# Optimization experiments

Hardware: AMD Instinct MI355X
Metric: run time of the kernel (lower is better)

Reference implementation:

```python
import jax, jax.numpy as jnp
import numpy as np

TEMPERATURE = 8.0  # sqrt(d_k), d_k = 64


def setup_inputs() -> dict:
    key = jax.random.key(0)
    kq, kk, kv = jax.random.split(key, 3)
    BH, N, D = 16, 4096, 64  # batch*heads, seq_len, head_dim
    q = jax.random.normal(kq, (BH, N, D), dtype=jnp.float32)
    k = jax.random.normal(kk, (BH, N, D), dtype=jnp.float32)
    v = jax.random.normal(kv, (BH, N, D), dtype=jnp.float32)
    # causal mask: True means masked (filled with -inf), broadcast over BH
    mask = jnp.triu(jnp.ones((N, N), dtype=jnp.bool_), k=1)[None, :, :]
    return {"q": q, "k": k, "v": v, "mask": mask}


def reference(q, k, v, mask):
    # attn = q @ k^T / temperature, masked softmax, attn @ v
    scores = jnp.einsum("bnd,bmd->bnm", q, k) / TEMPERATURE
    scores = jnp.where(mask, -jnp.inf, scores)
    attn = jax.nn.softmax(scores, axis=-1)  # dropout p=0 (eval) -> identity
    out = jnp.einsum("bnm,bmd->bnd", attn, v)
    return out, attn
```

## Files before the change

kernel.cpp:

```cpp
#include <hip/hip_runtime.h>

typedef float f32x4 __attribute__((ext_vector_type(4)));
typedef __bf16 bf16x8 __attribute__((ext_vector_type(8)));
typedef unsigned short u16x8 __attribute__((ext_vector_type(8)));
typedef unsigned int u32x4 __attribute__((ext_vector_type(4)));

#define NBH 16
#define NSEQ 4096
#define DH 64

__device__ __forceinline__ unsigned int cvtpk(float lo, float hi) {
  unsigned int r;
  asm("v_cvt_pk_bf16_f32 %0, %1, %2" : "=v"(r) : "v"(lo), "v"(hi));
  return r;
}
__device__ __forceinline__ bf16x8 pk8(const float* f) {
  union { unsigned int u[4]; bf16x8 b; } x;
#pragma unroll
  for (int i = 0; i < 4; ++i) x.u[i] = cvtpk(f[2 * i], f[2 * i + 1]);
  return x.b;
}

__device__ __forceinline__ void lbar() {
  __builtin_amdgcn_sched_barrier(0);
  asm volatile("s_waitcnt lgkmcnt(0)" ::: "memory");
  __builtin_amdgcn_s_barrier();
  __builtin_amdgcn_sched_barrier(0);
}

__global__ __launch_bounds__(512, 4) void sdpa_fused(
    const float* __restrict__ qg, const float* __restrict__ kg,
    const float* __restrict__ vg, float* __restrict__ outg) {
  const int bid = blockIdx.x;
  const int xcd = bid & 7;
  const int ii = bid >> 3;
  const int hh = ii >> 5;
  const int qt = ii & 31;
  const int b = 2 * xcd + hh;
  const int qa = qt, qb = 63 - qt;

  const int tid = threadIdx.x;
  const int w = tid >> 6, lane = tid & 63;
  const int g = lane >> 4, c = lane & 15;
  const int grp = w >> 2;
  const int wr0 = 16 * (w & 3);
  const int qrw = (grp ? qb : qa) * 64;
  const int kmax = grp ? qb : qa;
  const int pOff = 16 * w;

  const float* qbp = qg + (size_t)b * NSEQ * DH;
  const float* kbp = kg + (size_t)b * NSEQ * DH;
  const float* vbp = vg + (size_t)b * NSEQ * DH;
  float* outb = outg + (size_t)b * NSEQ * DH;
  float* attnb = outg + (size_t)NBH * NSEQ * DH + (size_t)b * NSEQ * NSEQ;

  __shared__ unsigned short Kl[2][64][72];
  __shared__ unsigned int Vt[2][64][37];
  __shared__ unsigned short Pl[128][72];

  bf16x8 aq[2];
  {
    const float* qrow = qbp + (size_t)(qrw + wr0 + c) * DH;
#pragma unroll
    for (int ks = 0; ks < 2; ++ks) {
      float f[8];
      *(float4*)f = *(const float4*)(qrow + 32 * ks + 8 * g);
      *(float4*)(f + 4) = *(const float4*)(qrow + 32 * ks + 8 * g + 4);
      aq[ks] = pk8(f);
    }
  }

  const int kj = tid >> 3, kcs = tid & 7;
  const int vp = tid >> 4, dch = tid & 15;
  float kf[8], vf0[4], vf1[4];

  auto loadK = [&](int kt) {
    const float* s = kbp + (size_t)(kt * 64 + kj) * DH + kcs * 8;
    *(float4*)kf = ((const float4*)s)[0];
    *(float4*)(kf + 4) = ((const float4*)s)[1];
  };
  auto writeK = [&](int cur) {
    u32x4 u;
#pragma unroll
    for (int i = 0; i < 4; ++i) u[i] = cvtpk(kf[2 * i], kf[2 * i + 1]);
    *(u32x4*)&Kl[cur][kj][kcs * 8] = u;
  };
  auto loadV = [&](int kt) {
    const float* s0 = vbp + (size_t)(kt * 64 + 2 * vp) * DH + dch * 4;
    *(float4*)vf0 = *(const float4*)s0;
    *(float4*)vf1 = *(const float4*)(s0 + DH);
  };
  auto writeV = [&](int cur) {
#pragma unroll
    for (int e = 0; e < 4; ++e) Vt[cur][4 * dch + e][vp] = cvtpk(vf0[e], vf1[e]);
  };

  float part[4] = {0.f, 0.f, 0.f, 0.f};
  loadK(0);
  for (int kt = 0; kt <= qb; ++kt) {
    const int cur = kt & 1;
    writeK(cur);
    lbar();
    if (kt < qb) loadK(kt + 1);
    if (kt <= kmax) {
      f32x4 acc[4];
#pragma unroll
      for (int ct = 0; ct < 4; ++ct) acc[ct] = (f32x4){0.f, 0.f, 0.f, 0.f};
#pragma unroll
      for (int ks = 0; ks < 2; ++ks)
#pragma unroll
        for (int ct = 0; ct < 4; ++ct) {
          u16x8 u = *(const u16x8*)&Kl[cur][16 * ct + c][32 * ks + 8 * g];
          acc[ct] = __builtin_amdgcn_mfma_f32_16x16x32_bf16(aq[ks], __builtin_bit_cast(bf16x8, u), acc[ct], 0, 0, 0);
        }
#pragma unroll
      for (int ct = 0; ct < 4; ++ct)
#pragma unroll
        for (int r = 0; r < 4; ++r) {
          const int j = kt * 64 + 16 * ct + c;
          const int i = qrw + wr0 + 4 * g + r;
          part[r] += (j <= i) ? __expf(acc[ct][r] * 0.125f) : 0.f;
        }
    }
  }
  float rinv[4];
#pragma unroll
  for (int r = 0; r < 4; ++r) {
    float s = part[r];
    s += __shfl_xor(s, 1); s += __shfl_xor(s, 2);
    s += __shfl_xor(s, 4); s += __shfl_xor(s, 8);
    rinv[r] = 1.f / s;
  }

  __syncthreads();

  loadK(0);
  loadV(0);
  f32x4 oacc[4];
#pragma unroll
  for (int ct = 0; ct < 4; ++ct) oacc[ct] = (f32x4){0.f, 0.f, 0.f, 0.f};

  for (int kt = 0; kt <= qb; ++kt) {
    const int cur = kt & 1;
    writeK(cur);
    writeV(cur);
    lbar();
    if (kt < qb) { loadK(kt + 1); loadV(kt + 1); }

    if (kt <= kmax) {
      f32x4 acc[4];
#pragma unroll
      for (int ct = 0; ct < 4; ++ct) acc[ct] = (f32x4){0.f, 0.f, 0.f, 0.f};
#pragma unroll
      for (int ks = 0; ks < 2; ++ks)
#pragma unroll
        for (int ct = 0; ct < 4; ++ct) {
          u16x8 u = *(const u16x8*)&Kl[cur][16 * ct + c][32 * ks + 8 * g];
          acc[ct] = __builtin_amdgcn_mfma_f32_16x16x32_bf16(aq[ks], __builtin_bit_cast(bf16x8, u), acc[ct], 0, 0, 0);
        }

#pragma unroll
      for (int ct = 0; ct < 4; ++ct)
#pragma unroll
        for (int r = 0; r < 4; ++r) {
          const int jl = 16 * ct + c;
          const int i = qrw + wr0 + 4 * g + r;
          const int j = kt * 64 + jl;
          const float p = (j <= i) ? __expf(acc[ct][r] * 0.125f) * rinv[r] : 0.f;
          Pl[pOff + 4 * g + r][jl] = (unsigned short)cvtpk(p, p);
          attnb[(size_t)i * NSEQ + j] = p;
        }

      bf16x8 ap[2];
#pragma unroll
      for (int ks = 0; ks < 2; ++ks)
        ap[ks] = __builtin_bit_cast(bf16x8, *(const u16x8*)&Pl[pOff + c][32 * ks + 8 * g]);
#pragma unroll
      for (int ks = 0; ks < 2; ++ks)
#pragma unroll
        for (int ct = 0; ct < 4; ++ct) {
          u16x8 bv = *(const u16x8*)&Vt[cur][16 * ct + c][16 * ks + 4 * g];
          oacc[ct] = __builtin_amdgcn_mfma_f32_16x16x32_bf16(ap[ks], __builtin_bit_cast(bf16x8, bv), oacc[ct], 0, 0, 0);
        }
    }
  }

#pragma unroll
  for (int ct = 0; ct < 4; ++ct)
#pragma unroll
    for (int r = 0; r < 4; ++r) {
      const int i = qrw + wr0 + 4 * g + r;
      outb[(size_t)i * DH + 16 * ct + c] = oacc[ct][r];
    }

  const float4 z = {0.f, 0.f, 0.f, 0.f};
#pragma unroll
  for (int t = 0; t < 2; ++t) {
    const int q0 = t ? qb : qa;
    const int zc0 = 64 * (q0 + 1);
    if (zc0 < NSEQ) {
      const int zw4 = (NSEQ - zc0) >> 2;
      for (int r = 0; r < 64; ++r) {
        float4* dst = (float4*)(attnb + (size_t)(q0 * 64 + r) * NSEQ + zc0);
        for (int c4 = tid; c4 < zw4; c4 += 512) dst[c4] = z;
      }
    }
  }
}

extern "C" void kernel_launch(void* const* d_in, const int* in_sizes, int n_in,
                              void* d_out, int out_size, void* d_ws, size_t ws_size,
                              hipStream_t stream) {
  (void)in_sizes; (void)n_in; (void)out_size; (void)d_ws; (void)ws_size;
  const float* q = (const float*)d_in[0];
  const float* k = (const float*)d_in[1];
  const float* v = (const float*)d_in[2];
  float* out = (float*)d_out;
  sdpa_fused<<<dim3(512), dim3(512), 0, stream>>>(q, k, v, out);
}
```

Baseline: 324.4 us.

## Interleave attention-matrix zero fill with the main loops and raise MFMA priority

The tail loop that writes zeros into the masked upper triangle of the attention output is replaced by an incremental fill state machine. A few fill steps run after each key tile in both passes, and whatever remains is drained at the end. This spreads the large store traffic across the compute phase so it overlaps with MFMA work instead of forming a serialized tail. s_setprio raises wave priority around the MFMA blocks. The cost is extra branching and scalar state per iteration, plus possible memory contention while the loops are running.

```diff
diff --git a/kernel.cpp b/kernel.cpp
--- a/kernel.cpp
+++ b/kernel.cpp
@@ -58,6 +58,34 @@
   __shared__ unsigned int Vt[2][64][37];
   __shared__ unsigned short Pl[128][72];
 
+  int fTile = 0;
+  int fq0 = qa;
+  int fzc4 = 16 * (qa + 1);
+  int fblk = fzc4 >> 6;
+  int fband = 0;
+  const int fr = tid >> 6, fc = tid & 63;
+  auto fillStep = [&]() {
+    if (fTile > 1) return;
+    const int r = fq0 * 64 + 4 * fband + fr;
+    const int c4 = fblk * 64 + fc;
+    if (c4 >= fzc4) {
+      const float4 z = {0.f, 0.f, 0.f, 0.f};
+      *(float4*)(attnb + (size_t)r * NSEQ + 4 * c4) = z;
+    }
+    if (++fband == 16) {
+      fband = 0;
+      if (++fblk == 16) {
+        if (fTile == 0) {
+          fTile = 1; fq0 = qb; fzc4 = 16 * (qb + 1); fblk = fzc4 >> 6; 
+          if (fblk >= 16) fTile = 2;
+        } else {
+          fTile = 2;
+        }
+      }
+    }
+  };
+  const int nfs = (qt >= 22) ? 4 : 3;
+
   bf16x8 aq[2];
   {
     const float* qrow = qbp + (size_t)(qrw + wr0 + c) * DH;
@@ -106,6 +134,7 @@
       f32x4 acc[4];
 #pragma unroll
       for (int ct = 0; ct < 4; ++ct) acc[ct] = (f32x4){0.f, 0.f, 0.f, 0.f};
+      __builtin_amdgcn_s_setprio(1);
 #pragma unroll
       for (int ks = 0; ks < 2; ++ks)
 #pragma unroll
@@ -113,6 +142,7 @@
           u16x8 u = *(const u16x8*)&Kl[cur][16 * ct + c][32 * ks + 8 * g];
           acc[ct] = __builtin_amdgcn_mfma_f32_16x16x32_bf16(aq[ks], __builtin_bit_cast(bf16x8, u), acc[ct], 0, 0, 0);
         }
+      __builtin_amdgcn_s_setprio(0);
 #pragma unroll
       for (int ct = 0; ct < 4; ++ct)
 #pragma unroll
@@ -122,6 +152,7 @@
           part[r] += (j <= i) ? __expf(acc[ct][r] * 0.125f) : 0.f;
         }
     }
+    for (int fs = 0; fs < nfs; ++fs) fillStep();
   }
   float rinv[4];
 #pragma unroll
@@ -151,6 +182,7 @@
       f32x4 acc[4];
 #pragma unroll
       for (int ct = 0; ct < 4; ++ct) acc[ct] = (f32x4){0.f, 0.f, 0.f, 0.f};
+      __builtin_amdgcn_s_setprio(1);
 #pragma unroll
       for (int ks = 0; ks < 2; ++ks)
 #pragma unroll
@@ -158,6 +190,7 @@
           u16x8 u = *(const u16x8*)&Kl[cur][16 * ct + c][32 * ks + 8 * g];
           acc[ct] = __builtin_amdgcn_mfma_f32_16x16x32_bf16(aq[ks], __builtin_bit_cast(bf16x8, u), acc[ct], 0, 0, 0);
         }
+      __builtin_amdgcn_s_setprio(0);
 
 #pragma unroll
       for (int ct = 0; ct < 4; ++ct)
@@ -175,6 +208,7 @@
 #pragma unroll
       for (int ks = 0; ks < 2; ++ks)
         ap[ks] = __builtin_bit_cast(bf16x8, *(const u16x8*)&Pl[pOff + c][32 * ks + 8 * g]);
+      __builtin_amdgcn_s_setprio(1);
 #pragma unroll
       for (int ks = 0; ks < 2; ++ks)
 #pragma unroll
@@ -182,7 +216,9 @@
           u16x8 bv = *(const u16x8*)&Vt[cur][16 * ct + c][16 * ks + 4 * g];
           oacc[ct] = __builtin_amdgcn_mfma_f32_16x16x32_bf16(ap[ks], __builtin_bit_cast(bf16x8, bv), oacc[ct], 0, 0, 0);
         }
-    }
+      __builtin_amdgcn_s_setprio(0);
+    }
+    for (int fs = 0; fs < nfs; ++fs) fillStep();
   }
 
 #pragma unroll
@@ -193,19 +229,7 @@
       outb[(size_t)i * DH + 16 * ct + c] = oacc[ct][r];
     }
 
-  const float4 z = {0.f, 0.f, 0.f, 0.f};
-#pragma unroll
-  for (int t = 0; t < 2; ++t) {
-    const int q0 = t ? qb : qa;
-    const int zc0 = 64 * (q0 + 1);
-    if (zc0 < NSEQ) {
-      const int zw4 = (NSEQ - zc0) >> 2;
-      for (int r = 0; r < 64; ++r) {
-        float4* dst = (float4*)(attnb + (size_t)(q0 * 64 + r) * NSEQ + zc0);
-        for (int c4 = tid; c4 < zw4; c4 += 512) dst[c4] = z;
-      }
-    }
-  }
+  while (fTile < 2) fillStep();
 }
 
 extern "C" void kernel_launch(void* const* d_in, const int* in_sizes, int n_in,
```

Measured after the change: 350.9 us. +8.2%, slower.

## Overlap attn zero-fill with pass one, read K directly, vectorize attn stores

Applied to the files above, without the earlier changes.

The first softmax-denominator pass now reads K straight from global memory into registers per wave, with no shared-memory staging or barriers, and runs only to each wave group's own causal limit. The masked-region zero-fill of the attention matrix is spread across that pass as coalesced float4 stores instead of being a tail loop. Attention probabilities are now written as 16-wide vector rows read back from the bf16 P tile in shared memory, instead of scattered scalar stores. Block-to-tile ordering is also changed. The trade-off is that stored attn values are rounded to bf16 rather than kept in fp32, and redundant global K reads replace shared reuse.

```diff
diff --git a/kernel.cpp b/kernel.cpp
--- a/kernel.cpp
+++ b/kernel.cpp
@@ -19,6 +19,9 @@
 #pragma unroll
   for (int i = 0; i < 4; ++i) x.u[i] = cvtpk(f[2 * i], f[2 * i + 1]);
   return x.b;
+}
+__device__ __forceinline__ float bf2f(unsigned short h) {
+  return __uint_as_float(((unsigned int)h) << 16);
 }
 
 __device__ __forceinline__ void lbar() {
@@ -35,7 +38,7 @@
   const int xcd = bid & 7;
   const int ii = bid >> 3;
   const int hh = ii >> 5;
-  const int qt = ii & 31;
+  const int qt = (ii < 32) ? ii : 63 - ii;
   const int b = 2 * xcd + hh;
   const int qa = qt, qb = 63 - qt;
 
@@ -70,6 +73,36 @@
     }
   }
 
+  auto qk_batch = [&](int kt, int ks, f32x4* acc) {
+    float4 ka[4], kb2[4];
+#pragma unroll
+    for (int ct = 0; ct < 4; ++ct) {
+      const float* s = kbp + (size_t)(kt * 64 + 16 * ct + c) * DH + 32 * ks + 8 * g;
+      ka[ct] = ((const float4*)s)[0];
+      kb2[ct] = ((const float4*)s)[1];
+    }
+#pragma unroll
+    for (int ct = 0; ct < 4; ++ct) {
+      float f[8];
+      *(float4*)f = ka[ct];
+      *(float4*)(f + 4) = kb2[ct];
+      acc[ct] = __builtin_amdgcn_mfma_f32_16x16x32_bf16(aq[ks], pk8(f), acc[ct], 0, 0, 0);
+    }
+  };
+
+  const int myChunk = 4 * w + g;
+  const int fc4 = c;
+  auto fillStep = [&](int s) {
+    const int cid = s * 32 + myChunk;
+    const int pr = cid / 63;
+    const int t = cid - pr * 63;
+    int row, col64;
+    if (t < 63 - qa) { row = qa * 64 + pr; col64 = qa + 1 + t; }
+    else             { row = qb * 64 + pr; col64 = t + 1; }
+    const float4 z = {0.f, 0.f, 0.f, 0.f};
+    *(float4*)(attnb + (size_t)row * NSEQ + col64 * 64 + fc4 * 4) = z;
+  };
+
   const int kj = tid >> 3, kcs = tid & 7;
   const int vp = tid >> 4, dch = tid & 15;
   float kf[8], vf0[4], vf1[4];
@@ -96,33 +129,25 @@
   };
 
   float part[4] = {0.f, 0.f, 0.f, 0.f};
-  loadK(0);
-  for (int kt = 0; kt <= qb; ++kt) {
-    const int cur = kt & 1;
-    writeK(cur);
-    lbar();
-    if (kt < qb) loadK(kt + 1);
-    if (kt <= kmax) {
-      f32x4 acc[4];
-#pragma unroll
-      for (int ct = 0; ct < 4; ++ct) acc[ct] = (f32x4){0.f, 0.f, 0.f, 0.f};
-#pragma unroll
-      for (int ks = 0; ks < 2; ++ks)
-#pragma unroll
-        for (int ct = 0; ct < 4; ++ct) {
-          u16x8 u = *(const u16x8*)&Kl[cur][16 * ct + c][32 * ks + 8 * g];
-          acc[ct] = __builtin_amdgcn_mfma_f32_16x16x32_bf16(aq[ks], __builtin_bit_cast(bf16x8, u), acc[ct], 0, 0, 0);
-        }
-#pragma unroll
-      for (int ct = 0; ct < 4; ++ct)
-#pragma unroll
-        for (int r = 0; r < 4; ++r) {
-          const int j = kt * 64 + 16 * ct + c;
-          const int i = qrw + wr0 + 4 * g + r;
-          part[r] += (j <= i) ? __expf(acc[ct][r] * 0.125f) : 0.f;
-        }
-    }
-  }
+  int fs = 0;
+  for (int kt = 0; kt <= kmax; ++kt) {
+    f32x4 acc[4];
+#pragma unroll
+    for (int ct = 0; ct < 4; ++ct) acc[ct] = (f32x4){0.f, 0.f, 0.f, 0.f};
+    qk_batch(kt, 0, acc);
+    if (fs < 126) { fillStep(fs); fillStep(fs + 1); fs += 2; }
+    qk_batch(kt, 1, acc);
+#pragma unroll
+    for (int ct = 0; ct < 4; ++ct)
+#pragma unroll
+      for (int r = 0; r < 4; ++r) {
+        const int j = kt * 64 + 16 * ct + c;
+        const int i = qrw + wr0 + 4 * g + r;
+        part[r] += (j <= i) ? __expf(acc[ct][r] * 0.125f) : 0.f;
+      }
+  }
+  while (fs < 126) { fillStep(fs); ++fs; }
+
   float rinv[4];
 #pragma unroll
   for (int r = 0; r < 4; ++r) {
@@ -131,8 +156,6 @@
     s += __shfl_xor(s, 4); s += __shfl_xor(s, 8);
     rinv[r] = 1.f / s;
   }
-
-  __syncthreads();
 
   loadK(0);
   loadV(0);
@@ -168,8 +191,21 @@
           const int j = kt * 64 + jl;
           const float p = (j <= i) ? __expf(acc[ct][r] * 0.125f) * rinv[r] : 0.f;
           Pl[pOff + 4 * g + r][jl] = (unsigned short)cvtpk(p, p);
-          attnb[(size_t)i * NSEQ + j] = p;
         }
+
+      {
+        const int lr = lane >> 2, lc = lane & 3;
+        u16x8 u0 = *(const u16x8*)&Pl[pOff + lr][lc * 16];
+        u16x8 u1 = *(const u16x8*)&Pl[pOff + lr][lc * 16 + 8];
+        float* dst = attnb + (size_t)(qrw + wr0 + lr) * NSEQ + kt * 64 + lc * 16;
+        float4 f0, f1, f2, f3;
+        f0.x = bf2f(u0[0]); f0.y = bf2f(u0[1]); f0.z = bf2f(u0[2]); f0.w = bf2f(u0[3]);
+        f1.x = bf2f(u0[4]); f1.y = bf2f(u0[5]); f1.z = bf2f(u0[6]); f1.w = bf2f(u0[7]);
+        f2.x = bf2f(u1[0]); f2.y = bf2f(u1[1]); f2.z = bf2f(u1[2]); f2.w = bf2f(u1[3]);
+        f3.x = bf2f(u1[4]); f3.y = bf2f(u1[5]); f3.z = bf2f(u1[6]); f3.w = bf2f(u1[7]);
+        ((float4*)dst)[0] = f0; ((float4*)dst)[1] = f1;
+        ((float4*)dst)[2] = f2; ((float4*)dst)[3] = f3;
+      }
 
       bf16x8 ap[2];
 #pragma unroll
@@ -192,20 +228,6 @@
       const int i = qrw + wr0 + 4 * g + r;
       outb[(size_t)i * DH + 16 * ct + c] = oacc[ct][r];
     }
-
-  const float4 z = {0.f, 0.f, 0.f, 0.f};
-#pragma unroll
-  for (int t = 0; t < 2; ++t) {
-    const int q0 = t ? qb : qa;
-    const int zc0 = 64 * (q0 + 1);
-    if (zc0 < NSEQ) {
-      const int zw4 = (NSEQ - zc0) >> 2;
-      for (int r = 0; r < 64; ++r) {
-        float4* dst = (float4*)(attnb + (size_t)(q0 * 64 + r) * NSEQ + zc0);
-        for (int c4 = tid; c4 < zw4; c4 += 512) dst[c4] = z;
-      }
-    }
-  }
 }
 
 extern "C" void kernel_launch(void* const* d_in, const int* in_sizes, int n_in,
```

Measured after the change: 491.9 us. +51.6%, slower.

## Split each key tile across wave halves and interleave causal zero-fill with compute

Applied to the files above, without the earlier changes.

Work is redistributed so that all 8 waves process the qa tile first and then the qb tile, with each half of the waves taking 32 of the 64 key columns. Before, the qa group sat idle while the qb group kept working. Partial row sums and output accumulators are merged across the two wave halves through a shared-memory union. The upper-triangle zero fill of attn is now spread across the loop iterations so those stores overlap compute. Attn is written through an LDS-staged, vectorized float4 path that stores the bf16-rounded probabilities, which changes the precision of the attn output. In exchange the kernel adds extra barriers and reduction traffic.

```diff
diff --git a/kernel.cpp b/kernel.cpp
--- a/kernel.cpp
+++ b/kernel.cpp
@@ -8,6 +8,7 @@
 #define NBH 16
 #define NSEQ 4096
 #define DH 64
+#define NST 65
 
 __device__ __forceinline__ unsigned int cvtpk(float lo, float hi) {
   unsigned int r;
@@ -20,7 +21,9 @@
   for (int i = 0; i < 4; ++i) x.u[i] = cvtpk(f[2 * i], f[2 * i + 1]);
   return x.b;
 }
-
+__device__ __forceinline__ float bf2f(unsigned short h) {
+  return __uint_as_float(((unsigned int)h) << 16);
+}
 __device__ __forceinline__ void lbar() {
   __builtin_amdgcn_sched_barrier(0);
   asm volatile("s_waitcnt lgkmcnt(0)" ::: "memory");
@@ -42,11 +45,10 @@
   const int tid = threadIdx.x;
   const int w = tid >> 6, lane = tid & 63;
   const int g = lane >> 4, c = lane & 15;
-  const int grp = w >> 2;
-  const int wr0 = 16 * (w & 3);
-  const int qrw = (grp ? qb : qa) * 64;
-  const int kmax = grp ? qb : qa;
-  const int pOff = 16 * w;
+  const int pw = w & 3, hf = w >> 2;
+  const int wr0 = 16 * pw;
+  const int ct0 = 2 * hf;
+  const int jb0 = 32 * hf;
 
   const float* qbp = qg + (size_t)b * NSEQ * DH;
   const float* kbp = kg + (size_t)b * NSEQ * DH;
@@ -54,19 +56,29 @@
   float* outb = outg + (size_t)b * NSEQ * DH;
   float* attnb = outg + (size_t)NBH * NSEQ * DH + (size_t)b * NSEQ * NSEQ;
 
-  __shared__ unsigned short Kl[2][64][72];
-  __shared__ unsigned int Vt[2][64][37];
-  __shared__ unsigned short Pl[128][72];
-
-  bf16x8 aq[2];
+  __shared__ union {
+    struct {
+      unsigned short Kl[2][64][72];
+      unsigned int Vt[2][64][37];
+      unsigned short Pl[64][72];
+    } m;
+    float ex[2][8][64];
+    float mg[4][64][16];
+  } sm;
+
+  bf16x8 aqA[2], aqB[2];
   {
-    const float* qrow = qbp + (size_t)(qrw + wr0 + c) * DH;
+    const float* ra = qbp + (size_t)(qa * 64 + wr0 + c) * DH;
+    const float* rb = qbp + (size_t)(qb * 64 + wr0 + c) * DH;
 #pragma unroll
     for (int ks = 0; ks < 2; ++ks) {
       float f[8];
-      *(float4*)f = *(const float4*)(qrow + 32 * ks + 8 * g);
-      *(float4*)(f + 4) = *(const float4*)(qrow + 32 * ks + 8 * g + 4);
-      aq[ks] = pk8(f);
+      *(float4*)f = *(const float4*)(ra + 32 * ks + 8 * g);
+      *(float4*)(f + 4) = *(const float4*)(ra + 32 * ks + 8 * g + 4);
+      aqA[ks] = pk8(f);
+      *(float4*)f = *(const float4*)(rb + 32 * ks + 8 * g);
+      *(float4*)(f + 4) = *(const float4*)(rb + 32 * ks + 8 * g + 4);
+      aqB[ks] = pk8(f);
     }
   }
 
@@ -83,7 +95,7 @@
     u32x4 u;
 #pragma unroll
     for (int i = 0; i < 4; ++i) u[i] = cvtpk(kf[2 * i], kf[2 * i + 1]);
-    *(u32x4*)&Kl[cur][kj][kcs * 8] = u;
+    *(u32x4*)&sm.m.Kl[cur][kj][kcs * 8] = u;
   };
   auto loadV = [&](int kt) {
     const float* s0 = vbp + (size_t)(kt * 64 + 2 * vp) * DH + dch * 4;
@@ -92,120 +104,228 @@
   };
   auto writeV = [&](int cur) {
 #pragma unroll
-    for (int e = 0; e < 4; ++e) Vt[cur][4 * dch + e][vp] = cvtpk(vf0[e], vf1[e]);
-  };
-
-  float part[4] = {0.f, 0.f, 0.f, 0.f};
+    for (int e = 0; e < 4; ++e) sm.m.Vt[cur][4 * dch + e][vp] = cvtpk(vf0[e], vf1[e]);
+  };
+
+  const int myChunk = 4 * w + g;
+  auto fillStep = [&](int s) {
+    const unsigned cid = (unsigned)(s * 32 + myChunk);
+    const unsigned pr = cid / 63u;
+    const int t = (int)(cid - pr * 63u);
+    int row, col64;
+    if (t < 63 - qa) { row = qa * 64 + (int)pr; col64 = qa + 1 + t; }
+    else             { row = qb * 64 + (int)pr; col64 = t + 1; }
+    const float4 z = {0.f, 0.f, 0.f, 0.f};
+    *(float4*)(attnb + (size_t)row * NSEQ + col64 * 64 + c * 4) = z;
+  };
+
+  float partA[4] = {0.f, 0.f, 0.f, 0.f};
+  float partB[4] = {0.f, 0.f, 0.f, 0.f};
   loadK(0);
-  for (int kt = 0; kt <= qb; ++kt) {
-    const int cur = kt & 1;
+  int fs = 0;
+  for (int s = 0; s < NST; ++s) {
+    const int cur = s & 1;
     writeK(cur);
     lbar();
-    if (kt < qb) loadK(kt + 1);
-    if (kt <= kmax) {
-      f32x4 acc[4];
-#pragma unroll
-      for (int ct = 0; ct < 4; ++ct) acc[ct] = (f32x4){0.f, 0.f, 0.f, 0.f};
+    if (s + 1 < NST) loadK((s + 1 <= qa) ? (s + 1) : (s - qa));
+    if (fs < 126) { fillStep(fs); fillStep(fs + 1); fs += 2; }
+
+    const bool isB = s > qa;
+    const int kt = isB ? s - qa - 1 : s;
+    f32x4 acc[2];
+    acc[0] = (f32x4){0.f, 0.f, 0.f, 0.f};
+    acc[1] = (f32x4){0.f, 0.f, 0.f, 0.f};
+    if (isB) {
 #pragma unroll
       for (int ks = 0; ks < 2; ++ks)
 #pragma unroll
-        for (int ct = 0; ct < 4; ++ct) {
-          u16x8 u = *(const u16x8*)&Kl[cur][16 * ct + c][32 * ks + 8 * g];
-          acc[ct] = __builtin_amdgcn_mfma_f32_16x16x32_bf16(aq[ks], __builtin_bit_cast(bf16x8, u), acc[ct], 0, 0, 0);
-        }
-#pragma unroll
-      for (int ct = 0; ct < 4; ++ct)
+        for (int cc = 0; cc < 2; ++cc) {
+          u16x8 u = *(const u16x8*)&sm.m.Kl[cur][16 * (ct0 + cc) + c][32 * ks + 8 * g];
+          acc[cc] = __builtin_amdgcn_mfma_f32_16x16x32_bf16(aqB[ks], __builtin_bit_cast(bf16x8, u), acc[cc], 0, 0, 0);
+        }
+#pragma unroll
+      for (int cc = 0; cc < 2; ++cc)
 #pragma unroll
         for (int r = 0; r < 4; ++r) {
-          const int j = kt * 64 + 16 * ct + c;
-          const int i = qrw + wr0 + 4 * g + r;
-          part[r] += (j <= i) ? __expf(acc[ct][r] * 0.125f) : 0.f;
-        }
-    }
-  }
-  float rinv[4];
+          const int j = kt * 64 + 16 * (ct0 + cc) + c;
+          const int i = qb * 64 + wr0 + 4 * g + r;
+          partB[r] += (j <= i) ? __expf(acc[cc][r] * 0.125f) : 0.f;
+        }
+    } else {
+#pragma unroll
+      for (int ks = 0; ks < 2; ++ks)
+#pragma unroll
+        for (int cc = 0; cc < 2; ++cc) {
+          u16x8 u = *(const u16x8*)&sm.m.Kl[cur][16 * (ct0 + cc) + c][32 * ks + 8 * g];
+          acc[cc] = __builtin_amdgcn_mfma_f32_16x16x32_bf16(aqA[ks], __builtin_bit_cast(bf16x8, u), acc[cc], 0, 0, 0);
+        }
+#pragma unroll
+      for (int cc = 0; cc < 2; ++cc)
+#pragma unroll
+        for (int r = 0; r < 4; ++r) {
+          const int j = kt * 64 + 16 * (ct0 + cc) + c;
+          const int i = qa * 64 + wr0 + 4 * g + r;
+          partA[r] += (j <= i) ? __expf(acc[cc][r] * 0.125f) : 0.f;
+        }
+    }
+  }
+
 #pragma unroll
   for (int r = 0; r < 4; ++r) {
-    float s = part[r];
-    s += __shfl_xor(s, 1); s += __shfl_xor(s, 2);
-    s += __shfl_xor(s, 4); s += __shfl_xor(s, 8);
-    rinv[r] = 1.f / s;
-  }
-
-  __syncthreads();
+    float sA = partA[r], sB = partB[r];
+    sA += __shfl_xor(sA, 1); sA += __shfl_xor(sA, 2);
+    sA += __shfl_xor(sA, 4); sA += __shfl_xor(sA, 8);
+    sB += __shfl_xor(sB, 1); sB += __shfl_xor(sB, 2);
+    sB += __shfl_xor(sB, 4); sB += __shfl_xor(sB, 8);
+    partA[r] = sA; partB[r] = sB;
+  }
 
   loadK(0);
   loadV(0);
-  f32x4 oacc[4];
-#pragma unroll
-  for (int ct = 0; ct < 4; ++ct) oacc[ct] = (f32x4){0.f, 0.f, 0.f, 0.f};
-
-  for (int kt = 0; kt <= qb; ++kt) {
-    const int cur = kt & 1;
+
+  __syncthreads();
+  if (c == 0) {
+#pragma unroll
+    for (int r = 0; r < 4; ++r) {
+      sm.ex[0][w][wr0 + 4 * g + r] = partA[r];
+      sm.ex[1][w][wr0 + 4 * g + r] = partB[r];
+    }
+  }
+  __syncthreads();
+  float rinvA[4], rinvB[4];
+#pragma unroll
+  for (int r = 0; r < 4; ++r) {
+    rinvA[r] = 1.f / (partA[r] + sm.ex[0][w ^ 4][wr0 + 4 * g + r]);
+    rinvB[r] = 1.f / (partB[r] + sm.ex[1][w ^ 4][wr0 + 4 * g + r]);
+  }
+  __syncthreads();
+
+  f32x4 oA[4], oB[4];
+#pragma unroll
+  for (int ct = 0; ct < 4; ++ct) {
+    oA[ct] = (f32x4){0.f, 0.f, 0.f, 0.f};
+    oB[ct] = (f32x4){0.f, 0.f, 0.f, 0.f};
+  }
+
+  for (int s = 0; s < NST; ++s) {
+    const int cur = s & 1;
     writeK(cur);
     writeV(cur);
     lbar();
-    if (kt < qb) { loadK(kt + 1); loadV(kt + 1); }
-
-    if (kt <= kmax) {
-      f32x4 acc[4];
-#pragma unroll
-      for (int ct = 0; ct < 4; ++ct) acc[ct] = (f32x4){0.f, 0.f, 0.f, 0.f};
+    if (s + 1 < NST) {
+      const int nk = (s + 1 <= qa) ? (s + 1) : (s - qa);
+      loadK(nk);
+      loadV(nk);
+    }
+
+    const bool isB = s > qa;
+    const int kt = isB ? s - qa - 1 : s;
+    const int qr0 = (isB ? qb : qa) * 64;
+
+    f32x4 acc[2];
+    acc[0] = (f32x4){0.f, 0.f, 0.f, 0.f};
+    acc[1] = (f32x4){0.f, 0.f, 0.f, 0.f};
+    if (isB) {
 #pragma unroll
       for (int ks = 0; ks < 2; ++ks)
 #pragma unroll
+        for (int cc = 0; cc < 2; ++cc) {
+          u16x8 u = *(const u16x8*)&sm.m.Kl[cur][16 * (ct0 + cc) + c][32 * ks + 8 * g];
+          acc[cc] = __builtin_amdgcn_mfma_f32_16x16x32_bf16(aqB[ks], __builtin_bit_cast(bf16x8, u), acc[cc], 0, 0, 0);
+        }
+#pragma unroll
+      for (int cc = 0; cc < 2; ++cc)
+#pragma unroll
+        for (int r = 0; r < 4; ++r) {
+          const int jl = 16 * (ct0 + cc) + c;
+          const int i = qr0 + wr0 + 4 * g + r;
+          const float p = (kt * 64 + jl <= i) ? __expf(acc[cc][r] * 0.125f) * rinvB[r] : 0.f;
+          sm.m.Pl[wr0 + 4 * g + r][jl] = (unsigned short)cvtpk(p, p);
+        }
+    } else {
+#pragma unroll
+      for (int ks = 0; ks < 2; ++ks)
+#pragma unroll
+        for (int cc = 0; cc < 2; ++cc) {
+          u16x8 u = *(const u16x8*)&sm.m.Kl[cur][16 * (ct0 + cc) + c][32 * ks + 8 * g];
+          acc[cc] = __builtin_amdgcn_mfma_f32_16x16x32_bf16(aqA[ks], __builtin_bit_cast(bf16x8, u), acc[cc], 0, 0, 0);
+        }
+#pragma unroll
+      for (int cc = 0; cc < 2; ++cc)
+#pragma unroll
+        for (int r = 0; r < 4; ++r) {
+          const int jl = 16 * (ct0 + cc) + c;
+          const int i = qr0 + wr0 + 4 * g + r;
+          const float p = (kt * 64 + jl <= i) ? __expf(acc[cc][r] * 0.125f) * rinvA[r] : 0.f;
+          sm.m.Pl[wr0 + 4 * g + r][jl] = (unsigned short)cvtpk(p, p);
+        }
+    }
+
+    {
+      const int lr = lane >> 2, lq = lane & 3;
+      u16x8 u = *(const u16x8*)&sm.m.Pl[wr0 + lr][jb0 + lq * 8];
+      float* dst = attnb + (size_t)(qr0 + wr0 + lr) * NSEQ + kt * 64 + jb0 + lq * 8;
+      float4 f0, f1;
+      f0.x = bf2f(u[0]); f0.y = bf2f(u[1]); f0.z = bf2f(u[2]); f0.w = bf2f(u[3]);
+      f1.x = bf2f(u[4]); f1.y = bf2f(u[5]); f1.z = bf2f(u[6]); f1.w = bf2f(u[7]);
+      ((float4*)dst)[0] = f0;
+      ((float4*)dst)[1] = f1;
+    }
+
+    {
+      bf16x8 ap = __builtin_bit_cast(bf16x8, *(const u16x8*)&sm.m.Pl[wr0 + c][jb0 + 8 * g]);
+      if (isB) {
+#pragma unroll
         for (int ct = 0; ct < 4; ++ct) {
-          u16x8 u = *(const u16x8*)&Kl[cur][16 * ct + c][32 * ks + 8 * g];
-          acc[ct] = __builtin_amdgcn_mfma_f32_16x16x32_bf16(aq[ks], __builtin_bit_cast(bf16x8, u), acc[ct], 0, 0, 0);
-        }
-
-#pragma unroll
-      for (int ct = 0; ct < 4; ++ct)
-#pragma unroll
-        for (int r = 0; r < 4; ++r) {
-          const int jl = 16 * ct + c;
-          const int i = qrw + wr0 + 4 * g + r;
-          const int j = kt * 64 + jl;
-          const float p = (j <= i) ? __expf(acc[ct][r] * 0.125f) * rinv[r] : 0.f;
-          Pl[pOff + 4 * g + r][jl] = (unsigned short)cvtpk(p, p);
-          attnb[(size_t)i * NSEQ + j] = p;
-        }
-
-      bf16x8 ap[2];
-#pragma unroll
-      for (int ks = 0; ks < 2; ++ks)
-        ap[ks] = __builtin_bit_cast(bf16x8, *(const u16x8*)&Pl[pOff + c][32 * ks + 8 * g]);
-#pragma unroll
-      for (int ks = 0; ks < 2; ++ks)
+          u16x8 bv = *(const u16x8*)&sm.m.Vt[cur][16 * ct + c][16 * hf + 4 * g];
+          oB[ct] = __builtin_amdgcn_mfma_f32_16x16x32_bf16(ap, __builtin_bit_cast(bf16x8, bv), oB[ct], 0, 0, 0);
+        }
+      } else {
 #pragma unroll
         for (int ct = 0; ct < 4; ++ct) {
-          u16x8 bv = *(const u16x8*)&Vt[cur][16 * ct + c][16 * ks + 4 * g];
-          oacc[ct] = __builtin_amdgcn_mfma_f32_16x16x32_bf16(ap[ks], __builtin_bit_cast(bf16x8, bv), oacc[ct], 0, 0, 0);
-        }
-    }
-  }
-
-#pragma unroll
-  for (int ct = 0; ct < 4; ++ct)
-#pragma unroll
-    for (int r = 0; r < 4; ++r) {
-      const int i = qrw + wr0 + 4 * g + r;
-      outb[(size_t)i * DH + 16 * ct + c] = oacc[ct][r];
-    }
-
-  const float4 z = {0.f, 0.f, 0.f, 0.f};
-#pragma unroll
-  for (int t = 0; t < 2; ++t) {
-    const int q0 = t ? qb : qa;
-    const int zc0 = 64 * (q0 + 1);
-    if (zc0 < NSEQ) {
-      const int zw4 = (NSEQ - zc0) >> 2;
-      for (int r = 0; r < 64; ++r) {
-        float4* dst = (float4*)(attnb + (size_t)(q0 * 64 + r) * NSEQ + zc0);
-        for (int c4 = tid; c4 < zw4; c4 += 512) dst[c4] = z;
+          u16x8 bv = *(const u16x8*)&sm.m.Vt[cur][16 * ct + c][16 * hf + 4 * g];
+          oA[ct] = __builtin_amdgcn_mfma_f32_16x16x32_bf16(ap, __builtin_bit_cast(bf16x8, bv), oA[ct], 0, 0, 0);
+        }
       }
     }
   }
+
+  __syncthreads();
+  if (hf) {
+#pragma unroll
+    for (int ct = 0; ct < 4; ++ct)
+#pragma unroll
+      for (int r = 0; r < 4; ++r) sm.mg[pw][lane][4 * ct + r] = oA[ct][r];
+  }
+  __syncthreads();
+  if (!hf) {
+#pragma unroll
+    for (int ct = 0; ct < 4; ++ct)
+#pragma unroll
+      for (int r = 0; r < 4; ++r) oA[ct][r] += sm.mg[pw][lane][4 * ct + r];
+  }
+  __syncthreads();
+  if (hf) {
+#pragma unroll
+    for (int ct = 0; ct < 4; ++ct)
+#pragma unroll
+      for (int r = 0; r < 4; ++r) sm.mg[pw][lane][4 * ct + r] = oB[ct][r];
+  }
+  __syncthreads();
+  if (!hf) {
+#pragma unroll
+    for (int ct = 0; ct < 4; ++ct)
+#pragma unroll
+      for (int r = 0; r < 4; ++r) {
+        oB[ct][r] += sm.mg[pw][lane][4 * ct + r];
+        const int ia = qa * 64 + wr0 + 4 * g + r;
+        const int ib = qb * 64 + wr0 + 4 * g + r;
+        outb[(size_t)ia * DH + 16 * ct + c] = oA[ct][r];
+        outb[(size_t)ib * DH + 16 * ct + c] = oB[ct][r];
+      }
+  }
+
+  while (fs < 126) { fillStep(fs); ++fs; }
 }
 
 extern "C" void kernel_launch(void* const* d_in, const int* in_sizes, int n_in,
```

After: 388.5 us. +19.7%, slower.
